# Optimization experiments

Hardware: AMD Instinct MI355X
Metric: run time of the kernel (lower is better)

Reference implementation:

```python
import jax, jax.numpy as jnp
import numpy as np

B, I, J, C, H = 1, 384, 384, 128, 4
CH = 128          # overall hidden
HD = CH // H      # 32 per head
INF = 1000000000.0
EPS = 1e-5


def setup_inputs() -> dict:
    key = jax.random.key(0)
    ks = jax.random.split(key, 10)
    s = 0.02
    return {
        "x": jax.random.normal(ks[0], (B, I, J, C), dtype=jnp.float32),
        "mask": jnp.ones((B, I, J), dtype=jnp.float32),
        "ln_w": jnp.ones((C,), dtype=jnp.float32),
        "ln_b": jnp.zeros((C,), dtype=jnp.float32),
        "wz": jax.random.normal(ks[1], (C, H), dtype=jnp.float32) * s,
        "bz": jnp.zeros((H,), dtype=jnp.float32),
        "wq": jax.random.normal(ks[2], (C, CH), dtype=jnp.float32) * s,
        "wk": jax.random.normal(ks[3], (C, CH), dtype=jnp.float32) * s,
        "wv": jax.random.normal(ks[4], (C, CH), dtype=jnp.float32) * s,
        "wg": jax.random.normal(ks[5], (C, CH), dtype=jnp.float32) * s,
        "bg": jnp.ones((CH,), dtype=jnp.float32),
        "wo": jax.random.normal(ks[6], (CH, C), dtype=jnp.float32) * s,
        "bo": jnp.zeros((C,), dtype=jnp.float32),
    }


def _layer_norm(x, w, b):
    mu = jnp.mean(x, axis=-1, keepdims=True)
    var = jnp.mean(jnp.square(x - mu), axis=-1, keepdims=True)
    return (x - mu) * jax.lax.rsqrt(var + EPS) * w + b


def reference(x, mask, ln_w, ln_b, wz, bz, wq, wk, wv, wg, bg, wo, bo):
    # starting=True: attention over last row axis J
    x = _layer_norm(x, ln_w, ln_b)                      # [B,I,J,C]
    mask_bias = (INF * (mask - 1.0))[:, :, None, None, :]   # [B,I,1,1,J]
    # triangle bias: linear_z then permute (2,0,1), unsqueeze(-4) -> [B,1,H,I,J]
    tri_bias = jnp.einsum("bijc,ch->bhij", x, wz) + bz[None, :, None, None]
    tri_bias = tri_bias[:, None]                        # [B,1,H,I,J]

    q = jnp.einsum("bijc,cd->bijd", x, wq).reshape(B, I, J, H, HD)
    k = jnp.einsum("bijc,cd->bijd", x, wk).reshape(B, I, J, H, HD)
    v = jnp.einsum("bijc,cd->bijd", x, wv).reshape(B, I, J, H, HD)
    q = q / jnp.sqrt(jnp.float32(HD))

    a = jnp.einsum("biqhd,bikhd->bihqk", q, k)          # [B,I,H,J,J]
    a = a + mask_bias + tri_bias
    a = jax.nn.softmax(a, axis=-1)
    o = jnp.einsum("bihqk,bikhd->biqhd", a, v)          # [B,I,J,H,HD]

    g = jax.nn.sigmoid(jnp.einsum("bijc,cd->bijd", x, wg) + bg)
    o = o.reshape(B, I, J, CH) * g
    return jnp.einsum("bijd,dc->bijc", o, wo) + bo      # [B,I,J,C]
```

## Files before the change

### kernel.cpp

```cpp
#include <hip/hip_runtime.h>
#include <math.h>

#define I_DIM 384
#define C_DIM 128
#define H_NUM 4
#define HD_DIM 32
#define M_DIM (I_DIM*I_DIM)
#define INF_F 1000000000.0f
#define EPS_F 1e-5f
#define QSCALE 0.17677669529663687f

typedef __attribute__((ext_vector_type(8))) short short8;
typedef __attribute__((ext_vector_type(4))) float f32x4;
union U4S8 { uint4 u; short8 s; };

__device__ __forceinline__ unsigned short f2bf(float f) {
    unsigned int u = __float_as_uint(f);
    u += 0x7fffu + ((u >> 16) & 1u);
    return (unsigned short)(u >> 16);
}
__device__ __forceinline__ float bf2f(unsigned short h) {
    return __uint_as_float((unsigned int)h << 16);
}
__device__ __forceinline__ unsigned int pk2(float a, float b) {
    return (unsigned int)f2bf(a) | ((unsigned int)f2bf(b) << 16);
}

__device__ uint4 wfmt_dev[5*4096];

__device__ __forceinline__ void load_lds16(const uint4* gp, void* lp) {
    __builtin_amdgcn_global_load_lds(
        (const __attribute__((address_space(1))) unsigned int*)gp,
        (__attribute__((address_space(3))) unsigned int*)lp,
        16, 0, 0);
}

__global__ __launch_bounds__(256) void wprep_kernel(
    const float* __restrict__ wq, const float* __restrict__ wk,
    const float* __restrict__ wg, const float* __restrict__ wv,
    const float* __restrict__ wo)
{
    const int tid  = blockIdx.x*256 + threadIdx.x;
    const int l    = tid & 63, tile = tid >> 6;
    const int ks   = tile & 3, nt = (tile >> 2) & 7;
    const int s    = (tile >> 5) & 1, m = tile >> 6;
    const float* W = (m==0)?wq:(m==1)?wk:(m==2)?wg:(m==3)?wv:wo;
    const float scale = (m==0) ? QSCALE : 1.f;
    const int n  = nt*16 + (l & 15);
    const int kb = ks*32 + (l >> 4)*8;
    unsigned int hw[4];
    #pragma unroll
    for (int jp = 0; jp < 4; ++jp) {
        unsigned short hs[2];
        #pragma unroll
        for (int e = 0; e < 2; ++e) {
            float v = W[(size_t)(kb + jp*2 + e)*C_DIM + n] * scale;
            unsigned short h = f2bf(v);
            if (s) h = f2bf(v - bf2f(h));
            hs[e] = h;
        }
        hw[jp] = (unsigned int)hs[0] | ((unsigned int)hs[1] << 16);
    }
    wfmt_dev[(size_t)m*4096 + (size_t)((s*8 + nt)*4 + ks)*64 + l] =
        make_uint4(hw[0], hw[1], hw[2], hw[3]);
}

__global__ __launch_bounds__(256, 4) void ln_proj_kernel(
    const float* __restrict__ x,
    const float* __restrict__ lnw, const float* __restrict__ lnb,
    const float* __restrict__ wz,  const float* __restrict__ bz,
    const float* __restrict__ bg,
    float* __restrict__ qo, unsigned short* __restrict__ ko16,
    unsigned int* __restrict__ vto, float* __restrict__ go,
    float* __restrict__ zo)
{
    __shared__ __align__(16) unsigned int xs[4096];
    __shared__ __align__(16) uint4 wbuf4[1024];
    unsigned int* vts = xs;

    const int t    = threadIdx.x;
    const int row0 = blockIdx.x * 64;
    const int w = t >> 6, l = t & 63, n16 = l & 15, quad = l >> 4;

    #pragma unroll
    for (int it = 0; it < 4; ++it) {
        const int tl = w*4 + it;
        const int s = tl >> 3, ntl = (tl >> 2) & 1, ks = tl & 3;
        load_lds16(wfmt_dev + (size_t)((s*8 + ntl)*4 + ks)*64 + l,
                   (char*)wbuf4 + tl*1024);
    }

    float4 xv[8];
    const int r = t >> 2, qt = t & 3, c0 = qt * 32;
    const int sw = (r & 7) << 2;
    {
        const float* xrow = x + (size_t)(row0 + r)*C_DIM + c0;
        float s = 0.f, ss = 0.f;
        #pragma unroll
        for (int i2 = 0; i2 < 8; i2++) {
            xv[i2] = ((const float4*)xrow)[i2];
            s  += xv[i2].x + xv[i2].y + xv[i2].z + xv[i2].w;
            ss += xv[i2].x*xv[i2].x + xv[i2].y*xv[i2].y
                + xv[i2].z*xv[i2].z + xv[i2].w*xv[i2].w;
        }
        s  += __shfl_xor(s, 1);  s  += __shfl_xor(s, 2);
        ss += __shfl_xor(ss, 1); ss += __shfl_xor(ss, 2);
        const float mean = s * (1.f/128.f);
        const float var  = ss * (1.f/128.f) - mean*mean;
        const float rstd = rsqrtf(var + EPS_F);
        const float4* wz4 = (const float4*)wz;
        float4 zacc = make_float4(0.f,0.f,0.f,0.f);
        #pragma unroll
        for (int i2 = 0; i2 < 8; i2++) {
            float4 w4 = ((const float4*)(lnw + c0))[i2];
            float4 b4 = ((const float4*)(lnb + c0))[i2];
            float4 r4;
            r4.x = (xv[i2].x - mean)*rstd*w4.x + b4.x;
            r4.y = (xv[i2].y - mean)*rstd*w4.y + b4.y;
            r4.z = (xv[i2].z - mean)*rstd*w4.z + b4.z;
            r4.w = (xv[i2].w - mean)*rstd*w4.w + b4.w;
            const float4 za = wz4[c0 + i2*4 + 0];
            const float4 zb_ = wz4[c0 + i2*4 + 1];
            const float4 zc = wz4[c0 + i2*4 + 2];
            const float4 zd = wz4[c0 + i2*4 + 3];
            zacc.x += r4.x*za.x + r4.y*zb_.x + r4.z*zc.x + r4.w*zd.x;
            zacc.y += r4.x*za.y + r4.y*zb_.y + r4.z*zc.y + r4.w*zd.y;
            zacc.z += r4.x*za.z + r4.y*zb_.z + r4.z*zc.z + r4.w*zd.z;
            zacc.w += r4.x*za.w + r4.y*zb_.w + r4.z*zc.w + r4.w*zd.w;
            const int wi = r*64 + qt*16 + i2*2;
            xs[(wi  ) ^ sw] = pk2(r4.x, r4.y);
            xs[(wi+1) ^ sw] = pk2(r4.z, r4.w);
            xv[i2] = r4;
        }
        zacc.x += __shfl_xor(zacc.x, 1); zacc.x += __shfl_xor(zacc.x, 2);
        zacc.y += __shfl_xor(zacc.y, 1); zacc.y += __shfl_xor(zacc.y, 2);
        zacc.z += __shfl_xor(zacc.z, 1); zacc.z += __shfl_xor(zacc.z, 2);
        zacc.w += __shfl_xor(zacc.w, 1); zacc.w += __shfl_xor(zacc.w, 2);
        const float zv = (qt==0)?zacc.x:(qt==1)?zacc.y:(qt==2)?zacc.z:zacc.w;
        zo[(size_t)qt*M_DIM + row0 + r] = zv + bz[qt];
    }
    __syncthreads();

    U4S8 ah[4], al[4];
    const int arow = w*16 + n16;
    #pragma unroll
    for (int ks = 0; ks < 4; ++ks) {
        const int bofs = arow*256 + ((ks*64 + quad*16) ^ ((arow & 7) << 4));
        ah[ks].u = *(const uint4*)((const char*)xs + bofs);
    }
    __syncthreads();

    #pragma unroll
    for (int i2 = 0; i2 < 8; i2++) {
        const float4 r4 = xv[i2];
        const unsigned short h0 = f2bf(r4.x), h1 = f2bf(r4.y),
                             h2 = f2bf(r4.z), h3 = f2bf(r4.w);
        const int wi = r*64 + qt*16 + i2*2;
        xs[(wi  ) ^ sw] = (unsigned int)f2bf(r4.x - bf2f(h0))
                        | ((unsigned int)f2bf(r4.y - bf2f(h1)) << 16);
        xs[(wi+1) ^ sw] = (unsigned int)f2bf(r4.z - bf2f(h2))
                        | ((unsigned int)f2bf(r4.w - bf2f(h3)) << 16);
    }
    __syncthreads();
    #pragma unroll
    for (int ks = 0; ks < 4; ++ks) {
        const int bofs = arow*256 + ((ks*64 + quad*16) ^ ((arow & 7) << 4));
        al[ks].u = *(const uint4*)((const char*)xs + bofs);
    }

    const int i_blk = row0 / I_DIM;
    const int jp0   = (row0 % I_DIM) >> 1;
    const int rw0   = row0 + w*16 + quad*4;

    #pragma unroll
    for (int rd = 0; rd < 16; ++rd) {
        const int mi = rd >> 2, qq = rd & 3;

        f32x4 acc[2];
        #pragma unroll
        for (int ntl = 0; ntl < 2; ++ntl) {
            f32x4 a = {0.f, 0.f, 0.f, 0.f};
            #pragma unroll
            for (int ks = 0; ks < 4; ++ks) {
                U4S8 bh, bl;
                bh.u = wbuf4[(    ntl*4 + ks)*64 + l];
                bl.u = wbuf4[(8 + ntl*4 + ks)*64 + l];
                a = __builtin_amdgcn_mfma_f32_16x16x32_bf16(ah[ks].s, bh.s, a, 0,0,0);
                a = __builtin_amdgcn_mfma_f32_16x16x32_bf16(al[ks].s, bh.s, a, 0,0,0);
                a = __builtin_amdgcn_mfma_f32_16x16x32_bf16(ah[ks].s, bl.s, a, 0,0,0);
            }
            acc[ntl] = a;
        }

        if (mi == 0) {
            #pragma unroll
            for (int ntl = 0; ntl < 2; ++ntl)
                #pragma unroll
                for (int rr = 0; rr < 4; ++rr)
                    qo[(size_t)(rw0 + rr)*C_DIM + qq*32 + ntl*16 + n16] =
                        acc[ntl][rr];
        } else if (mi == 1) {
            #pragma unroll
            for (int ntl = 0; ntl < 2; ++ntl)
                #pragma unroll
                for (int rr = 0; rr < 4; ++rr)
                    ko16[(size_t)(rw0 + rr)*C_DIM + qq*32 + ntl*16 + n16] =
                        f2bf(acc[ntl][rr]);
        } else if (mi == 2) {
            #pragma unroll
            for (int ntl = 0; ntl < 2; ++ntl) {
                const float bgv = bg[qq*32 + ntl*16 + n16];
                #pragma unroll
                for (int rr = 0; rr < 4; ++rr)
                    go[(size_t)(rw0 + rr)*C_DIM + qq*32 + ntl*16 + n16] =
                        1.f/(1.f + __expf(-(acc[ntl][rr] + bgv)));
            }
        } else {
            #pragma unroll
            for (int ntl = 0; ntl < 2; ++ntl)
                #pragma unroll
                for (int pr = 0; pr < 2; ++pr)
                    vts[(ntl*16 + n16)*33 + w*8 + quad*2 + pr] =
                        pk2(acc[ntl][2*pr], acc[ntl][2*pr+1]);
            __syncthreads();
            for (int idx = t; idx < 32*32; idx += 256) {
                const int ch_l = idx >> 5, p = idx & 31;
                vto[((size_t)i_blk*C_DIM + qq*32 + ch_l)*192 + jp0 + p] =
                    vts[ch_l*33 + p];
            }
        }

        __syncthreads();
        if (rd < 15) {
            const int m2 = (rd+1) >> 2, q2 = (rd+1) & 3;
            #pragma unroll
            for (int it = 0; it < 4; ++it) {
                const int tl = w*4 + it;
                const int s = tl >> 3, ntl2 = (tl >> 2) & 1, ks = tl & 3;
                load_lds16(wfmt_dev + (size_t)m2*4096
                           + (size_t)((s*8 + (q2*2 + ntl2))*4 + ks)*64 + l,
                           (char*)wbuf4 + tl*1024);
            }
        }
        __syncthreads();
    }
}

__global__ __launch_bounds__(256, 2) void attn_mfma_kernel(
    const float* q, const unsigned short* __restrict__ k16,
    const unsigned int* __restrict__ vt32, const float* __restrict__ zb,
    const float* __restrict__ mask, float* o)
{
    __shared__ uint4 Ks4[384*4];
    __shared__ uint4 VTl[32*49];
    __shared__ unsigned int PbU[4*784];
    __shared__ float mbl[384];

    const int ii = blockIdx.x;
    const int h  = blockIdx.y;
    const int t  = threadIdx.x;
    const size_t rbase = (size_t)ii*I_DIM*C_DIM + h*HD_DIM;

    for (int idx = t; idx < 1536; idx += 256) {
        const int j = idx >> 2, c4 = idx & 3;
        Ks4[j*4 + c4] = ((const uint4*)k16)[rbase/8 + (size_t)j*16 + c4];
    }
    for (int idx = t; idx < 1536; idx += 256) {
        const int d = idx / 48, m = idx - d*48;
        VTl[d*49 + m] = ((const uint4*)vt32)[((size_t)ii*C_DIM + h*HD_DIM + d)*48 + m];
    }
    for (int jj = t; jj < 384; jj += 256)
        mbl[jj] = INF_F * (mask[(size_t)ii*I_DIM + jj] - 1.f);
    __syncthreads();

    const int w = t >> 6, l = t & 63;
    const int n16 = l & 15, quad = l >> 4;

    #pragma unroll 1
    for (int qt = 0; qt < 6; qt++) {
        const int qg = w*6 + qt;

        U4S8 a;
        {
            const float* qrow = q + rbase + (size_t)(qg*16 + n16)*C_DIM + quad*8;
            const float4 f0 = ((const float4*)qrow)[0];
            const float4 f1 = ((const float4*)qrow)[1];
            a.u = make_uint4(pk2(f0.x,f0.y), pk2(f0.z,f0.w),
                             pk2(f1.x,f1.y), pk2(f1.z,f1.w));
        }

        f32x4 oacc0 = {0.f,0.f,0.f,0.f}, oacc1 = {0.f,0.f,0.f,0.f};
        float lsum[4] = {0.f, 0.f, 0.f, 0.f};
        const float* zbase = zb + (size_t)h*M_DIM
                           + (size_t)(qg*16 + quad*4)*I_DIM + n16;

        #pragma unroll 1
        for (int c = 0; c < 4; c++) {
            float zc[4][6];
            #pragma unroll
            for (int r = 0; r < 4; r++)
                #pragma unroll
                for (int k6 = 0; k6 < 6; k6++)
                    zc[r][k6] = zbase[(size_t)r*I_DIM + (6*c + k6)*16];
            float mbc[6];
            #pragma unroll
            for (int k6 = 0; k6 < 6; k6++)
                mbc[k6] = mbl[(6*c + k6)*16 + n16];

            f32x4 accS[6];
            #pragma unroll
            for (int k6 = 0; k6 < 6; k6++) {
                U4S8 b;
                b.u = Ks4[((6*c + k6)*16 + n16)*4 + quad];
                accS[k6] = __builtin_amdgcn_mfma_f32_16x16x32_bf16(
                    a.s, b.s, (f32x4){0.f,0.f,0.f,0.f}, 0, 0, 0);
            }

            #pragma unroll
            for (int r = 0; r < 4; r++)
                #pragma unroll
                for (int k6 = 0; k6 < 6; k6++) {
                    const float e = __expf(accS[k6][r] + mbc[k6] + zc[r][k6]);
                    accS[k6][r] = e;
                    lsum[r] += e;
                }

            #pragma unroll
            for (int k6 = 0; k6 < 6; k6++)
                #pragma unroll
                for (int r = 0; r < 4; r++) {
                    const float e  = accS[k6][r];
                    const float eo = __shfl_xor(e, 1);
                    if (!(l & 1))
                        PbU[w*784 + (quad*4+r)*49 + k6*8 + (n16 >> 1)] = pk2(e, eo);
                }

            #pragma unroll
            for (int km = 0; km < 3; km++) {
                const int pbase = w*784 + n16*49 + quad*4 + 16*km;
                U4S8 pa;
                pa.u = make_uint4(PbU[pbase], PbU[pbase+1], PbU[pbase+2], PbU[pbase+3]);
                U4S8 vb0, vb1;
                vb0.u = VTl[(n16     )*49 + quad + 4*km + 12*c];
                vb1.u = VTl[(16 + n16)*49 + quad + 4*km + 12*c];
                oacc0 = __builtin_amdgcn_mfma_f32_16x16x32_bf16(pa.s, vb0.s, oacc0, 0,0,0);
                oacc1 = __builtin_amdgcn_mfma_f32_16x16x32_bf16(pa.s, vb1.s, oacc1, 0,0,0);
            }
        }

        #pragma unroll
        for (int r = 0; r < 4; r++) {
            float s_ = lsum[r];
            s_ += __shfl_xor(s_, 1);
            s_ += __shfl_xor(s_, 2);
            s_ += __shfl_xor(s_, 4);
            s_ += __shfl_xor(s_, 8);
            const float rcp = 1.f / s_;
            const size_t orow = rbase + (size_t)(qg*16 + quad*4 + r)*C_DIM;
            o[orow + n16]      = oacc0[r] * rcp;
            o[orow + 16 + n16] = oacc1[r] * rcp;
        }
    }
}

__global__ __launch_bounds__(256, 4) void out_proj_kernel(
    const float* __restrict__ o, const float* g,
    const float* __restrict__ bo, float* out)
{
    __shared__ __align__(16) unsigned int xs[4096];
    __shared__ __align__(16) uint4 wbuf4[1024];
    const int t    = threadIdx.x;
    const int row0 = blockIdx.x * 64;
    const int w = t >> 6, l = t & 63, n16 = l & 15, quad = l >> 4;

    #pragma unroll
    for (int it = 0; it < 4; ++it) {
        const int tl = w*4 + it;
        const int s = tl >> 3, ntl = (tl >> 2) & 1, ks = tl & 3;
        load_lds16(wfmt_dev + (size_t)4*4096 + (size_t)((s*8 + ntl)*4 + ks)*64 + l,
                   (char*)wbuf4 + tl*1024);
    }

    float4 pv[8];
    const int r = t >> 2, qt = t & 3, c0 = qt * 32;
    const int sw = (r & 7) << 2;
    {
        const float4* orow = (const float4*)(o + (size_t)(row0 + r)*C_DIM + c0);
        const float4* grow = (const float4*)(g + (size_t)(row0 + r)*C_DIM + c0);
        #pragma unroll
        for (int i2 = 0; i2 < 8; i2++) {
            const float4 a = orow[i2];
            const float4 b = grow[i2];
            float4 p;
            p.x = a.x*b.x; p.y = a.y*b.y; p.z = a.z*b.z; p.w = a.w*b.w;
            const int wi = r*64 + qt*16 + i2*2;
            xs[(wi  ) ^ sw] = pk2(p.x, p.y);
            xs[(wi+1) ^ sw] = pk2(p.z, p.w);
            pv[i2] = p;
        }
    }
    __syncthreads();

    U4S8 ah[4], al[4];
    const int arow = w*16 + n16;
    #pragma unroll
    for (int ks = 0; ks < 4; ++ks) {
        const int bofs = arow*256 + ((ks*64 + quad*16) ^ ((arow & 7) << 4));
        ah[ks].u = *(const uint4*)((const char*)xs + bofs);
    }
    __syncthreads();
    #pragma unroll
    for (int i2 = 0; i2 < 8; i2++) {
        const float4 p = pv[i2];
        const unsigned short h0 = f2bf(p.x), h1 = f2bf(p.y),
                             h2 = f2bf(p.z), h3 = f2bf(p.w);
        const int wi = r*64 + qt*16 + i2*2;
        xs[(wi  ) ^ sw] = (unsigned int)f2bf(p.x - bf2f(h0))
                        | ((unsigned int)f2bf(p.y - bf2f(h1)) << 16);
        xs[(wi+1) ^ sw] = (unsigned int)f2bf(p.z - bf2f(h2))
                        | ((unsigned int)f2bf(p.w - bf2f(h3)) << 16);
    }
    __syncthreads();
    #pragma unroll
    for (int ks = 0; ks < 4; ++ks) {
        const int bofs = arow*256 + ((ks*64 + quad*16) ^ ((arow & 7) << 4));
        al[ks].u = *(const uint4*)((const char*)xs + bofs);
    }

    const int rw0 = row0 + w*16 + quad*4;
    #pragma unroll
    for (int qq = 0; qq < 4; ++qq) {
        f32x4 acc[2];
        #pragma unroll
        for (int ntl = 0; ntl < 2; ++ntl) {
            f32x4 a = {0.f, 0.f, 0.f, 0.f};
            #pragma unroll
            for (int ks = 0; ks < 4; ++ks) {
                U4S8 bh, bl;
                bh.u = wbuf4[(    ntl*4 + ks)*64 + l];
                bl.u = wbuf4[(8 + ntl*4 + ks)*64 + l];
                a = __builtin_amdgcn_mfma_f32_16x16x32_bf16(ah[ks].s, bh.s, a, 0,0,0);
                a = __builtin_amdgcn_mfma_f32_16x16x32_bf16(al[ks].s, bh.s, a, 0,0,0);
                a = __builtin_amdgcn_mfma_f32_16x16x32_bf16(ah[ks].s, bl.s, a, 0,0,0);
            }
            acc[ntl] = a;
        }
        #pragma unroll
        for (int ntl = 0; ntl < 2; ++ntl) {
            const int n = qq*32 + ntl*16 + n16;
            const float bov = bo[n];
            #pragma unroll
            for (int rr = 0; rr < 4; ++rr)
                out[(size_t)(rw0 + rr)*C_DIM + n] = acc[ntl][rr] + bov;
        }
        __syncthreads();
        if (qq < 3) {
            const int q2 = qq + 1;
            #pragma unroll
            for (int it = 0; it < 4; ++it) {
                const int tl = w*4 + it;
                const int s = tl >> 3, ntl2 = (tl >> 2) & 1, ks = tl & 3;
                load_lds16(wfmt_dev + (size_t)4*4096
                           + (size_t)((s*8 + (q2*2 + ntl2))*4 + ks)*64 + l,
                           (char*)wbuf4 + tl*1024);
            }
        }
        __syncthreads();
    }
}

extern "C" void kernel_launch(void* const* d_in, const int* in_sizes, int n_in,
                              void* d_out, int out_size, void* d_ws, size_t ws_size,
                              hipStream_t stream)
{
    (void)in_sizes; (void)n_in; (void)out_size; (void)ws_size;
    const float* x    = (const float*)d_in[0];
    const float* mask = (const float*)d_in[1];
    const float* lnw  = (const float*)d_in[2];
    const float* lnb  = (const float*)d_in[3];
    const float* wz   = (const float*)d_in[4];
    const float* bz   = (const float*)d_in[5];
    const float* wq   = (const float*)d_in[6];
    const float* wk   = (const float*)d_in[7];
    const float* wv   = (const float*)d_in[8];
    const float* wg   = (const float*)d_in[9];
    const float* bg   = (const float*)d_in[10];
    const float* wo   = (const float*)d_in[11];
    const float* bo   = (const float*)d_in[12];

    float* ws = (float*)d_ws;
    float* qb   = ws;
    float* zbuf = qb + (size_t)M_DIM*C_DIM;
    unsigned short* kb16 = (unsigned short*)(zbuf + (size_t)H_NUM*M_DIM);
    unsigned int*   vt32 = (unsigned int*)(kb16 + (size_t)M_DIM*C_DIM);
    float* gbuf = (float*)d_out;

    wprep_kernel<<<80, 256, 0, stream>>>(wq, wk, wg, wv, wo);
    ln_proj_kernel<<<M_DIM/64, 256, 0, stream>>>(
        x, lnw, lnb, wz, bz, bg, qb, kb16, vt32, gbuf, zbuf);
    attn_mfma_kernel<<<dim3(I_DIM, H_NUM), 256, 0, stream>>>(
        qb, kb16, vt32, zbuf, mask, qb );
    out_proj_kernel<<<M_DIM/64, 256, 0, stream>>>(
        qb, gbuf, bo, (float*)d_out);
}
```

Before: 500.0 us.

## Transpose attention MFMA operands to keep P in registers via shuffles

```diff
diff --git a/kernel.cpp b/kernel.cpp
--- a/kernel.cpp
+++ b/kernel.cpp
@@ -24,6 +24,11 @@
 }
 __device__ __forceinline__ unsigned int pk2(float a, float b) {
     return (unsigned int)f2bf(a) | ((unsigned int)f2bf(b) << 16);
+}
+__device__ __forceinline__ unsigned int cvtpk(float lo, float hi) {
+    unsigned int r;
+    asm("v_cvt_pk_bf16_f32 %0, %1, %2" : "=v"(r) : "v"(lo), "v"(hi));
+    return r;
 }
 
 __device__ uint4 wfmt_dev[5*4096];
@@ -246,15 +251,14 @@
     }
 }
 
-__global__ __launch_bounds__(256, 2) void attn_mfma_kernel(
+__global__ __launch_bounds__(256, 3) void attn_mfma_kernel(
     const float* q, const unsigned short* __restrict__ k16,
     const unsigned int* __restrict__ vt32, const float* __restrict__ zb,
     const float* __restrict__ mask, float* o)
 {
     __shared__ uint4 Ks4[384*4];
     __shared__ uint4 VTl[32*49];
-    __shared__ unsigned int PbU[4*784];
-    __shared__ float mbl[384];
+    __shared__ __align__(16) float mbl[384];
 
     const int ii = blockIdx.x;
     const int h  = blockIdx.y;
@@ -263,7 +267,8 @@
 
     for (int idx = t; idx < 1536; idx += 256) {
         const int j = idx >> 2, c4 = idx & 3;
-        Ks4[j*4 + c4] = ((const uint4*)k16)[rbase/8 + (size_t)j*16 + c4];
+        Ks4[j*4 + (c4 ^ ((j >> 1) & 3))] =
+            ((const uint4*)k16)[rbase/8 + (size_t)j*16 + c4];
     }
     for (int idx = t; idx < 1536; idx += 256) {
         const int d = idx / 48, m = idx - d*48;
@@ -275,6 +280,9 @@
 
     const int w = t >> 6, l = t & 63;
     const int n16 = l & 15, quad = l >> 4;
+    const int slA = n16 + ((quad & 1) << 5);
+    const int slB = slA + 16;
+    const bool hi = (quad & 2) != 0;
 
     #pragma unroll 1
     for (int qt = 0; qt < 6; qt++) {
@@ -285,81 +293,79 @@
             const float* qrow = q + rbase + (size_t)(qg*16 + n16)*C_DIM + quad*8;
             const float4 f0 = ((const float4*)qrow)[0];
             const float4 f1 = ((const float4*)qrow)[1];
-            a.u = make_uint4(pk2(f0.x,f0.y), pk2(f0.z,f0.w),
-                             pk2(f1.x,f1.y), pk2(f1.z,f1.w));
+            a.u = make_uint4(cvtpk(f0.x,f0.y), cvtpk(f0.z,f0.w),
+                             cvtpk(f1.x,f1.y), cvtpk(f1.z,f1.w));
         }
 
         f32x4 oacc0 = {0.f,0.f,0.f,0.f}, oacc1 = {0.f,0.f,0.f,0.f};
-        float lsum[4] = {0.f, 0.f, 0.f, 0.f};
-        const float* zbase = zb + (size_t)h*M_DIM
-                           + (size_t)(qg*16 + quad*4)*I_DIM + n16;
+        float lsum = 0.f;
+        const float* zrow = zb + (size_t)h*M_DIM
+                          + (size_t)(qg*16 + n16)*I_DIM + quad*4;
 
         #pragma unroll 1
         for (int c = 0; c < 4; c++) {
-            float zc[4][6];
-            #pragma unroll
-            for (int r = 0; r < 4; r++)
-                #pragma unroll
-                for (int k6 = 0; k6 < 6; k6++)
-                    zc[r][k6] = zbase[(size_t)r*I_DIM + (6*c + k6)*16];
-            float mbc[6];
+            float4 zc4[6];
             #pragma unroll
             for (int k6 = 0; k6 < 6; k6++)
-                mbc[k6] = mbl[(6*c + k6)*16 + n16];
+                zc4[k6] = *(const float4*)&zrow[96*c + k6*16];
+            float4 mb4[6];
+            #pragma unroll
+            for (int k6 = 0; k6 < 6; k6++)
+                mb4[k6] = *(const float4*)&mbl[96*c + k6*16 + quad*4];
 
             f32x4 accS[6];
             #pragma unroll
             for (int k6 = 0; k6 < 6; k6++) {
+                const int key = (6*c + k6)*16 + n16;
                 U4S8 b;
-                b.u = Ks4[((6*c + k6)*16 + n16)*4 + quad];
+                b.u = Ks4[key*4 + (quad ^ ((key >> 1) & 3))];
                 accS[k6] = __builtin_amdgcn_mfma_f32_16x16x32_bf16(
-                    a.s, b.s, (f32x4){0.f,0.f,0.f,0.f}, 0, 0, 0);
-            }
-
-            #pragma unroll
-            for (int r = 0; r < 4; r++)
-                #pragma unroll
-                for (int k6 = 0; k6 < 6; k6++) {
-                    const float e = __expf(accS[k6][r] + mbc[k6] + zc[r][k6]);
-                    accS[k6][r] = e;
-                    lsum[r] += e;
-                }
-
-            #pragma unroll
-            for (int k6 = 0; k6 < 6; k6++)
-                #pragma unroll
-                for (int r = 0; r < 4; r++) {
-                    const float e  = accS[k6][r];
-                    const float eo = __shfl_xor(e, 1);
-                    if (!(l & 1))
-                        PbU[w*784 + (quad*4+r)*49 + k6*8 + (n16 >> 1)] = pk2(e, eo);
-                }
+                    b.s, a.s, (f32x4){0.f,0.f,0.f,0.f}, 0, 0, 0);
+            }
+
+            unsigned int pu[6][2];
+            #pragma unroll
+            for (int k6 = 0; k6 < 6; k6++) {
+                const float e0 = __expf(accS[k6][0] + zc4[k6].x + mb4[k6].x);
+                const float e1 = __expf(accS[k6][1] + zc4[k6].y + mb4[k6].y);
+                const float e2 = __expf(accS[k6][2] + zc4[k6].z + mb4[k6].z);
+                const float e3 = __expf(accS[k6][3] + zc4[k6].w + mb4[k6].w);
+                lsum += (e0 + e1) + (e2 + e3);
+                pu[k6][0] = cvtpk(e0, e1);
+                pu[k6][1] = cvtpk(e2, e3);
+            }
 
             #pragma unroll
             for (int km = 0; km < 3; km++) {
-                const int pbase = w*784 + n16*49 + quad*4 + 16*km;
+                const unsigned int x0 = __shfl((int)pu[2*km  ][0], slA);
+                const unsigned int x1 = __shfl((int)pu[2*km+1][0], slA);
+                const unsigned int y0 = __shfl((int)pu[2*km  ][1], slA);
+                const unsigned int y1 = __shfl((int)pu[2*km+1][1], slA);
+                const unsigned int z0 = __shfl((int)pu[2*km  ][0], slB);
+                const unsigned int z1 = __shfl((int)pu[2*km+1][0], slB);
+                const unsigned int w0 = __shfl((int)pu[2*km  ][1], slB);
+                const unsigned int w1 = __shfl((int)pu[2*km+1][1], slB);
                 U4S8 pa;
-                pa.u = make_uint4(PbU[pbase], PbU[pbase+1], PbU[pbase+2], PbU[pbase+3]);
+                pa.u = make_uint4(hi?x1:x0, hi?y1:y0, hi?z1:z0, hi?w1:w0);
                 U4S8 vb0, vb1;
                 vb0.u = VTl[(n16     )*49 + quad + 4*km + 12*c];
                 vb1.u = VTl[(16 + n16)*49 + quad + 4*km + 12*c];
-                oacc0 = __builtin_amdgcn_mfma_f32_16x16x32_bf16(pa.s, vb0.s, oacc0, 0,0,0);
-                oacc1 = __builtin_amdgcn_mfma_f32_16x16x32_bf16(pa.s, vb1.s, oacc1, 0,0,0);
-            }
-        }
-
-        #pragma unroll
-        for (int r = 0; r < 4; r++) {
-            float s_ = lsum[r];
-            s_ += __shfl_xor(s_, 1);
-            s_ += __shfl_xor(s_, 2);
-            s_ += __shfl_xor(s_, 4);
-            s_ += __shfl_xor(s_, 8);
-            const float rcp = 1.f / s_;
-            const size_t orow = rbase + (size_t)(qg*16 + quad*4 + r)*C_DIM;
-            o[orow + n16]      = oacc0[r] * rcp;
-            o[orow + 16 + n16] = oacc1[r] * rcp;
-        }
+                oacc0 = __builtin_amdgcn_mfma_f32_16x16x32_bf16(vb0.s, pa.s, oacc0, 0,0,0);
+                oacc1 = __builtin_amdgcn_mfma_f32_16x16x32_bf16(vb1.s, pa.s, oacc1, 0,0,0);
+            }
+        }
+
+        float s_ = lsum;
+        s_ += __shfl_xor(s_, 16);
+        s_ += __shfl_xor(s_, 32);
+        const float rcp = 1.f / s_;
+        const size_t orow = rbase + (size_t)(qg*16 + n16)*C_DIM;
+        float4 o0 = make_float4(oacc0[0]*rcp, oacc0[1]*rcp,
+                                oacc0[2]*rcp, oacc0[3]*rcp);
+        float4 o1 = make_float4(oacc1[0]*rcp, oacc1[1]*rcp,
+                                oacc1[2]*rcp, oacc1[3]*rcp);
+        *(float4*)&o[orow + quad*4]      = o0;
+        *(float4*)&o[orow + 16 + quad*4] = o1;
     }
 }
 
```

Measured after the change: 440.9 us. 1.13x faster.
